# Performance work log

Measured on AMD Instinct MI355X. Metric: run time of the kernel, lower is better.

## Reference

```python
import jax, jax.numpy as jnp
import numpy as np

EPS_NORM = 1e-12  # matches torch F.normalize eps
EPS_LOG = 1e-10


def _l2norm(x):
    n = jnp.sqrt(jnp.sum(x * x, axis=-1, keepdims=True))
    return x / jnp.maximum(n, EPS_NORM)


def setup_inputs() -> dict:
    key = jax.random.key(0)
    k1, k2 = jax.random.split(key)
    B, H, K, Dh = 65536, 4, 512, 256
    z_e = jax.random.normal(k1, (B, H * Dh), dtype=jnp.float32)
    emb = jax.random.normal(k2, (H, K, Dh), dtype=jnp.float32)  # per-head codebooks
    logit_scales = jnp.ones((H,), dtype=jnp.float32) * 10.0
    return {"z_e": z_e, "emb": emb, "logit_scales": logit_scales}


def reference(z_e, emb, logit_scales):
    B = z_e.shape[0]
    H, K, Dh = emb.shape
    z = z_e.reshape(B, H, Dh)
    zn = _l2norm(z)                      # [B,H,Dh]
    en = _l2norm(emb)                    # [H,K,Dh]
    # per-head cosine similarity, scaled
    logits = logit_scales[None, :, None] * jnp.einsum('bhd,hkd->bhk', zn, en)  # [B,H,K]
    idx = jnp.argmax(logits, axis=-1)    # [B,H] int
    # embedding gather per head: emb[h, idx[b,h]] -> [B,H,Dh]
    z_q = emb[jnp.arange(H)[None, :], idx].reshape(B, H * Dh)
    # perplexity per head
    probs = jax.nn.softmax(logits, axis=-1)          # [B,H,K]
    avg_probs = probs.mean(axis=0)                   # [H,K]
    perp = jnp.exp(-jnp.sum(avg_probs * jnp.log(avg_probs + EPS_LOG), axis=-1))  # [H]
    avg_perplexity = perp.mean()
    # combined radix index over heads
    combined = idx[:, 0]
    for h in range(1, H):
        combined = combined * K + idx[:, h]
    return z_q, combined, avg_perplexity
```

## Files before the change

kernel.cpp:

```cpp
#include <hip/hip_runtime.h>
#include <stdint.h>
#include <math.h>

#define BT   65536
#define H    4
#define K    512
#define DH   256
#define EPSN 1e-12f
#define EPSL 1e-10f
#define TAU  0.03f
#define CTH  0.970446f
#define CMAX 16
#define NREP 8
#define LOG2E 1.4426950408889634f

typedef short bf16x8 __attribute__((ext_vector_type(8)));
typedef float f32x4  __attribute__((ext_vector_type(4)));

__device__ inline unsigned short f2bf(float f) {
  uint32_t u = __builtin_bit_cast(uint32_t, f);
  u += 0x7fffu + ((u >> 16) & 1u);
  return (unsigned short)(u >> 16);
}

__device__ inline uint32_t pack_bf2(float lo, float hi) {
  uint32_t r;
  asm("v_cvt_pk_bf16_f32 %0, %1, %2" : "=v"(r) : "v"(lo), "v"(hi));
  return r;
}


__global__ __launch_bounds__(256) void vq_prep(const float* __restrict__ emb,
                                               const float* __restrict__ scales,
                                               float* __restrict__ en_f,
                                               unsigned short* __restrict__ en_t,
                                               float* __restrict__ avgp) {
  const int hk = blockIdx.x;
  const int t  = threadIdx.x;
  const float v = emb[(size_t)hk * DH + t];
  float s = v * v;
#pragma unroll
  for (int m = 1; m < 64; m <<= 1) s += __shfl_xor(s, m);
  __shared__ float wsum[4];
  if ((t & 63) == 0) wsum[t >> 6] = s;
  __syncthreads();
  const float tot = wsum[0] + wsum[1] + wsum[2] + wsum[3];
  const float n   = fmaxf(sqrtf(tot), EPSN);
  const float vn  = v / n;
  en_f[(size_t)hk * DH + t] = vn;

  const int h    = hk >> 9, k = hk & (K - 1);
  const float s2 = scales[h] * LOG2E;
  const int kblk = k >> 4, arow = k & 15;
  const int ks   = t >> 5, kg = (t >> 3) & 3, e = t & 7;
  const int lane = (kg << 4) | arow;
  en_t[(((size_t)(h * 32 + kblk) * 8 + ks) * 64 + lane) * 8 + e] = f2bf(vn * s2);
  if (t < NREP) avgp[t * (H * K) + hk] = 0.0f;
}

__global__ __launch_bounds__(512, 4) void vq_main(
    const float* __restrict__ z_e, const float* __restrict__ emb,
    const float* __restrict__ en_f, const unsigned short* __restrict__ en_t,
    float* __restrict__ avgp, int* __restrict__ idx_ws,
    float* __restrict__ outq) {
  const int h     = blockIdx.y;
  const int bbase = blockIdx.x * 64;
  const int t     = threadIdx.x;
  const int w     = t >> 6;
  const int l     = t & 63;
  const int arow  = l & 15;
  const int kg    = l >> 4;

  __shared__ unsigned short a_lds[64 * 256];
  __shared__ float norms[64];
  __shared__ float invn_l[64];
  __shared__ float wredm[8][64];
  __shared__ float wreds[8][64];
  __shared__ __align__(16) unsigned short cand[64][CMAX];
  __shared__ float thr[64];
  __shared__ float Srec[64];
  __shared__ int   cnt[64];
  __shared__ float avg_lds[512];

  {
    const int row = t >> 3;
    const int c8  = t & 7;
    const float* zp = z_e + (size_t)(bbase + row) * (H * DH) + h * DH;
    float4 q[8];
    float ss = 0.0f;
    const int swz = (row & 7) << 4;
#pragma unroll
    for (int j = 0; j < 8; j++) {
      q[j] = *(const float4*)(zp + c8 * 4 + j * 32);
      const int d = c8 * 4 + j * 32;
      uint2 pk;
      pk.x = pack_bf2(q[j].x, q[j].y);
      pk.y = pack_bf2(q[j].z, q[j].w);
      *(uint2*)((char*)a_lds + row * 512 + ((d * 2) ^ swz)) = pk;
      ss += q[j].x * q[j].x + q[j].y * q[j].y + q[j].z * q[j].z + q[j].w * q[j].w;
    }
    ss += __shfl_xor(ss, 1);
    ss += __shfl_xor(ss, 2);
    ss += __shfl_xor(ss, 4);
    const float n = fmaxf(sqrtf(ss), EPSN);
    if (c8 == 0) { norms[row] = n; invn_l[row] = 1.0f / n; }
    if (t < 64) cnt[t] = 0;
  }

  const unsigned short* ep =
      en_t + (((size_t)(h * 32 + w * 4) * 8) * 64 + l) * 8;
  bf16x8 ef0[4];
#pragma unroll
  for (int mi = 0; mi < 4; mi++)
    ef0[mi] = *(const bf16x8*)(ep + (size_t)(mi * 8) * 512);

  __syncthreads();

  f32x4 acc[4][4];
#pragma unroll
  for (int mi = 0; mi < 4; mi++)
#pragma unroll
    for (int ni = 0; ni < 4; ni++) acc[mi][ni] = (f32x4){0.f, 0.f, 0.f, 0.f};

#pragma unroll
  for (int ks = 0; ks < 8; ks++) {
    bf16x8 ef[4];
    if (ks == 0) {
#pragma unroll
      for (int mi = 0; mi < 4; mi++) ef[mi] = ef0[mi];
    } else {
#pragma unroll
      for (int mi = 0; mi < 4; mi++)
        ef[mi] = *(const bf16x8*)(ep + (size_t)(mi * 8 + ks) * 512);
    }
    bf16x8 zf[4];
#pragma unroll
    for (int ni = 0; ni < 4; ni++) {
      const int rr = ni * 16 + arow;
      const int kb = (ks * 64) | (kg * 16);
      zf[ni] = *(const bf16x8*)((const char*)a_lds + rr * 512 +
                                (kb ^ ((rr & 7) << 4)));
    }
#pragma unroll
    for (int mi = 0; mi < 4; mi++)
#pragma unroll
      for (int ni = 0; ni < 4; ni++)
        acc[mi][ni] = __builtin_amdgcn_mfma_f32_16x16x32_bf16(ef[mi], zf[ni],
                                                              acc[mi][ni], 0, 0, 0);
  }

  float rn[4];
#pragma unroll
  for (int ni = 0; ni < 4; ni++) rn[ni] = invn_l[ni * 16 + arow];
  float m1[4], es[4];
#pragma unroll
  for (int ni = 0; ni < 4; ni++) { m1[ni] = 0.0f; es[ni] = 0.0f; }
#pragma unroll
  for (int mi = 0; mi < 4; mi++)
#pragma unroll
    for (int ni = 0; ni < 4; ni++)
#pragma unroll
      for (int q = 0; q < 4; q++) {
        const float e = __builtin_amdgcn_exp2f(acc[mi][ni][q] * rn[ni]);
        acc[mi][ni][q] = e;
        m1[ni] = fmaxf(m1[ni], e);
        es[ni] += e;
      }
#pragma unroll
  for (int m = 16; m < 64; m <<= 1) {
#pragma unroll
    for (int ni = 0; ni < 4; ni++) {
      m1[ni] = fmaxf(m1[ni], __shfl_xor(m1[ni], m));
      es[ni] += __shfl_xor(es[ni], m);
    }
  }
  if (kg == 0) {
#pragma unroll
    for (int ni = 0; ni < 4; ni++) {
      const int r = ni * 16 + arow;
      wredm[w][r] = m1[ni];
      wreds[w][r] = es[ni];
    }
  }
  __syncthreads();
  if (t < 64) {
    float a1 = 0.0f, s = 0.0f;
#pragma unroll
    for (int ww = 0; ww < 8; ww++) {
      a1 = fmaxf(a1, wredm[ww][t]);
      s += wreds[ww][t];
    }
    thr[t] = a1 * CTH; Srec[t] = 1.0f / s;
  }
  __syncthreads();

  {
    float rs[4], th[4];
#pragma unroll
    for (int ni = 0; ni < 4; ni++) {
      const int r = ni * 16 + arow;
      rs[ni] = Srec[r];
      th[ni] = thr[r];
    }
#pragma unroll
    for (int mi = 0; mi < 4; mi++)
#pragma unroll
      for (int q = 0; q < 4; q++) {
        float vs = 0.0f;
#pragma unroll
        for (int ni = 0; ni < 4; ni++) {
          const float e = acc[mi][ni][q];
          vs = fmaf(e, rs[ni], vs);
          if (e >= th[ni]) {
            const int r = ni * 16 + arow;
            const int p = atomicAdd(&cnt[r], 1);
            if (p < CMAX)
              cand[r][p] = (unsigned short)(w * 64 + mi * 16 + kg * 4 + q);
          }
        }
        vs += __shfl_xor(vs, 1);
        vs += __shfl_xor(vs, 2);
        vs += __shfl_xor(vs, 4);
        vs += __shfl_xor(vs, 8);
        if (arow == 0) avg_lds[w * 64 + mi * 16 + kg * 4 + q] = vs;
      }
  }
  __syncthreads();

  {
    float* ap = avgp + (blockIdx.x & (NREP - 1)) * (H * K) + h * K;
    atomicAdd(&ap[t], avg_lds[t]);
  }

  int best8[8];
#pragma unroll
  for (int i = 0; i < 8; i++) {
    const int r = w * 8 + i;
    int c = cnt[r];
    int best;
    if (c <= 1) {
      best = cand[r][0];
    } else {
      if (c > CMAX) c = CMAX;
      const float nrm = norms[r];
      const float4 zq = *(const float4*)(z_e + (size_t)(bbase + r) * (H * DH) +
                                         h * DH + l * 4);
      const float zn0 = zq.x / nrm, zn1 = zq.y / nrm,
                  zn2 = zq.z / nrm, zn3 = zq.w / nrm;
      float bv = -INFINITY; int bi = 1 << 30;
      for (int j = 0; j < c; j++) {
        const int cd = cand[r][j];
        const float4 eq = *(const float4*)(en_f + ((size_t)(h * K) + cd) * DH + l * 4);
        float d0 = fmaf(zn0, eq.x, fmaf(zn1, eq.y, fmaf(zn2, eq.z, zn3 * eq.w)));
#pragma unroll
        for (int m = 1; m < 64; m <<= 1) d0 += __shfl_xor(d0, m);
        if (d0 > bv || (d0 == bv && cd < bi)) { bv = d0; bi = cd; }
      }
      best = bi;
    }
    best8[i] = best;
    if (l == i) idx_ws[(size_t)(bbase + r) * H + h] = best;
  }

  {
    float4 gv[8];
#pragma unroll
    for (int i = 0; i < 8; i++)
      gv[i] = *(const float4*)(emb + ((size_t)(h * K) + best8[i]) * DH + l * 4);
#pragma unroll
    for (int i = 0; i < 8; i++)
      *(float4*)(outq + (size_t)(bbase + w * 8 + i) * (H * DH) + h * DH + l * 4) =
          gv[i];
  }
}

__global__ __launch_bounds__(256) void vq_tail(const int* __restrict__ idx_ws,
                                               const float* __restrict__ avgp,
                                               float* __restrict__ out_comb,
                                               float* __restrict__ out_perp) {
  const int t = threadIdx.x;
  if (blockIdx.x < 256) {
    const int b = blockIdx.x * 256 + t;
    const int* p = idx_ws + (size_t)b * H;
    uint32_t cv = (uint32_t)p[0];
    cv = cv * 512u + (uint32_t)p[1];
    cv = cv * 512u + (uint32_t)p[2];
    cv = cv * 512u + (uint32_t)p[3];
    out_comb[b] = (float)(int32_t)cv;
    return;
  }
  float sh[H] = {0.f, 0.f, 0.f, 0.f};
  for (int i = t; i < H * K; i += 256) {
    const int h = i >> 9;
    float a = 0.0f;
#pragma unroll
    for (int c = 0; c < NREP; c++) a += avgp[c * (H * K) + i];
    a /= 65536.0f;
    sh[h] += a * logf(a + EPSL);
  }
  __shared__ float red[4][H];
#pragma unroll
  for (int h = 0; h < H; h++) {
    float s = sh[h];
#pragma unroll
    for (int m = 1; m < 64; m <<= 1) s += __shfl_xor(s, m);
    if ((t & 63) == 0) red[t >> 6][h] = s;
  }
  __syncthreads();
  if (t == 0) {
    float p = 0.0f;
#pragma unroll
    for (int h = 0; h < H; h++) {
      const float s = red[0][h] + red[1][h] + red[2][h] + red[3][h];
      p += expf(-s);
    }
    out_perp[0] = p * 0.25f;
  }
}

extern "C" void kernel_launch(void* const* d_in, const int* in_sizes, int n_in,
                              void* d_out, int out_size, void* d_ws, size_t ws_size,
                              hipStream_t stream) {
  const float* z_e    = (const float*)d_in[0];
  const float* emb    = (const float*)d_in[1];
  const float* scales = (const float*)d_in[2];
  float* out = (float*)d_out;

  float*          en_f   = (float*)d_ws;
  unsigned short* en_t   = (unsigned short*)(en_f + (size_t)H * K * DH);
  float*          avgp   = (float*)(en_t + (size_t)H * K * DH);
  int*            idx_ws = (int*)(avgp + NREP * H * K);

  hipLaunchKernelGGL(vq_prep, dim3(H * K), dim3(256), 0, stream,
                     emb, scales, en_f, en_t, avgp);
  hipLaunchKernelGGL(vq_main, dim3(BT / 64, H), dim3(512), 0, stream,
                     z_e, emb, en_f, en_t, avgp, idx_ws, out);
  hipLaunchKernelGGL(vq_tail, dim3(BT / 256 + 1), dim3(256), 0, stream,
                     idx_ws, avgp, out + (size_t)BT * H * DH,
                     out + (size_t)BT * H * DH + BT);
}
```

Measured before the change: 225.0 us.

## Process two 64-row tiles per block to amortize setup and atomics

Each vq_main block now handles 128 rows as two 64-row tiles, and the grid is halved to match. The global loads of z for both tiles are issued up front so more memory traffic is in flight at once. The perplexity partial sums of both tiles are combined in LDS before a single atomic flush, which halves the global atomics. The cost is that the row tile, candidate and count LDS buffers are doubled, which may lower the number of resident blocks per CU, and the codebook fragments are re-read from memory for the second tile.

```diff
diff --git a/kernel.cpp b/kernel.cpp
--- a/kernel.cpp
+++ b/kernel.cpp
@@ -64,47 +64,65 @@
     float* __restrict__ avgp, int* __restrict__ idx_ws,
     float* __restrict__ outq) {
   const int h     = blockIdx.y;
-  const int bbase = blockIdx.x * 64;
+  const int bbase = blockIdx.x * 128;
   const int t     = threadIdx.x;
   const int w     = t >> 6;
   const int l     = t & 63;
   const int arow  = l & 15;
   const int kg    = l >> 4;
 
-  __shared__ unsigned short a_lds[64 * 256];
-  __shared__ float norms[64];
-  __shared__ float invn_l[64];
+  __shared__ unsigned short a_lds[2][64 * 256];
+  __shared__ float norms[2][64];
+  __shared__ float invn_l[2][64];
   __shared__ float wredm[8][64];
   __shared__ float wreds[8][64];
-  __shared__ __align__(16) unsigned short cand[64][CMAX];
+  __shared__ __align__(16) unsigned short cand[2][64][CMAX];
   __shared__ float thr[64];
   __shared__ float Srec[64];
-  __shared__ int   cnt[64];
+  __shared__ int   cnt[2][64];
   __shared__ float avg_lds[512];
 
   {
     const int row = t >> 3;
     const int c8  = t & 7;
-    const float* zp = z_e + (size_t)(bbase + row) * (H * DH) + h * DH;
-    float4 q[8];
-    float ss = 0.0f;
+    const float* zp0 = z_e + (size_t)(bbase + row) * (H * DH) + h * DH;
+    const float* zp1 = zp0 + (size_t)64 * (H * DH);
+    float4 q0[8], q1[8];
+#pragma unroll
+    for (int j = 0; j < 8; j++) q0[j] = *(const float4*)(zp0 + c8 * 4 + j * 32);
+#pragma unroll
+    for (int j = 0; j < 8; j++) q1[j] = *(const float4*)(zp1 + c8 * 4 + j * 32);
     const int swz = (row & 7) << 4;
+    float ss0 = 0.0f, ss1 = 0.0f;
 #pragma unroll
     for (int j = 0; j < 8; j++) {
-      q[j] = *(const float4*)(zp + c8 * 4 + j * 32);
       const int d = c8 * 4 + j * 32;
       uint2 pk;
-      pk.x = pack_bf2(q[j].x, q[j].y);
-      pk.y = pack_bf2(q[j].z, q[j].w);
-      *(uint2*)((char*)a_lds + row * 512 + ((d * 2) ^ swz)) = pk;
-      ss += q[j].x * q[j].x + q[j].y * q[j].y + q[j].z * q[j].z + q[j].w * q[j].w;
-    }
-    ss += __shfl_xor(ss, 1);
-    ss += __shfl_xor(ss, 2);
-    ss += __shfl_xor(ss, 4);
-    const float n = fmaxf(sqrtf(ss), EPSN);
-    if (c8 == 0) { norms[row] = n; invn_l[row] = 1.0f / n; }
-    if (t < 64) cnt[t] = 0;
+      pk.x = pack_bf2(q0[j].x, q0[j].y);
+      pk.y = pack_bf2(q0[j].z, q0[j].w);
+      *(uint2*)((char*)&a_lds[0][0] + row * 512 + ((d * 2) ^ swz)) = pk;
+      ss0 += q0[j].x * q0[j].x + q0[j].y * q0[j].y +
+             q0[j].z * q0[j].z + q0[j].w * q0[j].w;
+    }
+#pragma unroll
+    for (int j = 0; j < 8; j++) {
+      const int d = c8 * 4 + j * 32;
+      uint2 pk;
+      pk.x = pack_bf2(q1[j].x, q1[j].y);
+      pk.y = pack_bf2(q1[j].z, q1[j].w);
+      *(uint2*)((char*)&a_lds[1][0] + row * 512 + ((d * 2) ^ swz)) = pk;
+      ss1 += q1[j].x * q1[j].x + q1[j].y * q1[j].y +
+             q1[j].z * q1[j].z + q1[j].w * q1[j].w;
+    }
+    ss0 += __shfl_xor(ss0, 1); ss0 += __shfl_xor(ss0, 2); ss0 += __shfl_xor(ss0, 4);
+    ss1 += __shfl_xor(ss1, 1); ss1 += __shfl_xor(ss1, 2); ss1 += __shfl_xor(ss1, 4);
+    if (c8 == 0) {
+      const float n0 = fmaxf(sqrtf(ss0), EPSN);
+      const float n1 = fmaxf(sqrtf(ss1), EPSN);
+      norms[0][row] = n0; invn_l[0][row] = 1.0f / n0;
+      norms[1][row] = n1; invn_l[1][row] = 1.0f / n1;
+    }
+    if (t < 64) { cnt[0][t] = 0; cnt[1][t] = 0; }
   }
 
   const unsigned short* ep =
@@ -116,114 +134,120 @@
 
   __syncthreads();
 
-  f32x4 acc[4][4];
-#pragma unroll
-  for (int mi = 0; mi < 4; mi++)
-#pragma unroll
-    for (int ni = 0; ni < 4; ni++) acc[mi][ni] = (f32x4){0.f, 0.f, 0.f, 0.f};
-
-#pragma unroll
-  for (int ks = 0; ks < 8; ks++) {
-    bf16x8 ef[4];
-    if (ks == 0) {
-#pragma unroll
-      for (int mi = 0; mi < 4; mi++) ef[mi] = ef0[mi];
-    } else {
+#pragma unroll
+  for (int tile = 0; tile < 2; ++tile) {
+    const unsigned short* al = &a_lds[tile][0];
+
+    f32x4 acc[4][4];
+#pragma unroll
+    for (int mi = 0; mi < 4; mi++)
+#pragma unroll
+      for (int ni = 0; ni < 4; ni++) acc[mi][ni] = (f32x4){0.f, 0.f, 0.f, 0.f};
+
+#pragma unroll
+    for (int ks = 0; ks < 8; ks++) {
+      bf16x8 ef[4];
 #pragma unroll
       for (int mi = 0; mi < 4; mi++)
-        ef[mi] = *(const bf16x8*)(ep + (size_t)(mi * 8 + ks) * 512);
-    }
-    bf16x8 zf[4];
-#pragma unroll
-    for (int ni = 0; ni < 4; ni++) {
-      const int rr = ni * 16 + arow;
-      const int kb = (ks * 64) | (kg * 16);
-      zf[ni] = *(const bf16x8*)((const char*)a_lds + rr * 512 +
-                                (kb ^ ((rr & 7) << 4)));
-    }
+        ef[mi] = (tile == 0 && ks == 0)
+                     ? ef0[mi]
+                     : *(const bf16x8*)(ep + (size_t)(mi * 8 + ks) * 512);
+      bf16x8 zf[4];
+#pragma unroll
+      for (int ni = 0; ni < 4; ni++) {
+        const int rr = ni * 16 + arow;
+        const int kb = (ks * 64) | (kg * 16);
+        zf[ni] = *(const bf16x8*)((const char*)al + rr * 512 +
+                                  (kb ^ ((rr & 7) << 4)));
+      }
+#pragma unroll
+      for (int mi = 0; mi < 4; mi++)
+#pragma unroll
+        for (int ni = 0; ni < 4; ni++)
+          acc[mi][ni] = __builtin_amdgcn_mfma_f32_16x16x32_bf16(ef[mi], zf[ni],
+                                                                acc[mi][ni], 0, 0, 0);
+    }
+
+    float rn[4];
+#pragma unroll
+    for (int ni = 0; ni < 4; ni++) rn[ni] = invn_l[tile][ni * 16 + arow];
+    float m1[4], es[4];
+#pragma unroll
+    for (int ni = 0; ni < 4; ni++) { m1[ni] = 0.0f; es[ni] = 0.0f; }
 #pragma unroll
     for (int mi = 0; mi < 4; mi++)
 #pragma unroll
       for (int ni = 0; ni < 4; ni++)
-        acc[mi][ni] = __builtin_amdgcn_mfma_f32_16x16x32_bf16(ef[mi], zf[ni],
-                                                              acc[mi][ni], 0, 0, 0);
-  }
-
-  float rn[4];
-#pragma unroll
-  for (int ni = 0; ni < 4; ni++) rn[ni] = invn_l[ni * 16 + arow];
-  float m1[4], es[4];
-#pragma unroll
-  for (int ni = 0; ni < 4; ni++) { m1[ni] = 0.0f; es[ni] = 0.0f; }
-#pragma unroll
-  for (int mi = 0; mi < 4; mi++)
-#pragma unroll
-    for (int ni = 0; ni < 4; ni++)
-#pragma unroll
-      for (int q = 0; q < 4; q++) {
-        const float e = __builtin_amdgcn_exp2f(acc[mi][ni][q] * rn[ni]);
-        acc[mi][ni][q] = e;
-        m1[ni] = fmaxf(m1[ni], e);
-        es[ni] += e;
-      }
-#pragma unroll
-  for (int m = 16; m < 64; m <<= 1) {
-#pragma unroll
-    for (int ni = 0; ni < 4; ni++) {
-      m1[ni] = fmaxf(m1[ni], __shfl_xor(m1[ni], m));
-      es[ni] += __shfl_xor(es[ni], m);
-    }
-  }
-  if (kg == 0) {
-#pragma unroll
-    for (int ni = 0; ni < 4; ni++) {
-      const int r = ni * 16 + arow;
-      wredm[w][r] = m1[ni];
-      wreds[w][r] = es[ni];
-    }
-  }
-  __syncthreads();
-  if (t < 64) {
-    float a1 = 0.0f, s = 0.0f;
-#pragma unroll
-    for (int ww = 0; ww < 8; ww++) {
-      a1 = fmaxf(a1, wredm[ww][t]);
-      s += wreds[ww][t];
-    }
-    thr[t] = a1 * CTH; Srec[t] = 1.0f / s;
-  }
-  __syncthreads();
-
-  {
-    float rs[4], th[4];
-#pragma unroll
-    for (int ni = 0; ni < 4; ni++) {
-      const int r = ni * 16 + arow;
-      rs[ni] = Srec[r];
-      th[ni] = thr[r];
-    }
-#pragma unroll
-    for (int mi = 0; mi < 4; mi++)
-#pragma unroll
-      for (int q = 0; q < 4; q++) {
-        float vs = 0.0f;
-#pragma unroll
-        for (int ni = 0; ni < 4; ni++) {
-          const float e = acc[mi][ni][q];
-          vs = fmaf(e, rs[ni], vs);
-          if (e >= th[ni]) {
-            const int r = ni * 16 + arow;
-            const int p = atomicAdd(&cnt[r], 1);
-            if (p < CMAX)
-              cand[r][p] = (unsigned short)(w * 64 + mi * 16 + kg * 4 + q);
+#pragma unroll
+        for (int q = 0; q < 4; q++) {
+          const float e = __builtin_amdgcn_exp2f(acc[mi][ni][q] * rn[ni]);
+          acc[mi][ni][q] = e;
+          m1[ni] = fmaxf(m1[ni], e);
+          es[ni] += e;
+        }
+#pragma unroll
+    for (int m = 16; m < 64; m <<= 1) {
+#pragma unroll
+      for (int ni = 0; ni < 4; ni++) {
+        m1[ni] = fmaxf(m1[ni], __shfl_xor(m1[ni], m));
+        es[ni] += __shfl_xor(es[ni], m);
+      }
+    }
+    if (kg == 0) {
+#pragma unroll
+      for (int ni = 0; ni < 4; ni++) {
+        const int r = ni * 16 + arow;
+        wredm[w][r] = m1[ni];
+        wreds[w][r] = es[ni];
+      }
+    }
+    __syncthreads();
+    if (t < 64) {
+      float a1 = 0.0f, s = 0.0f;
+#pragma unroll
+      for (int ww = 0; ww < 8; ww++) {
+        a1 = fmaxf(a1, wredm[ww][t]);
+        s += wreds[ww][t];
+      }
+      thr[t] = a1 * CTH; Srec[t] = 1.0f / s;
+    }
+    __syncthreads();
+
+    {
+      float rs[4], th4[4];
+#pragma unroll
+      for (int ni = 0; ni < 4; ni++) {
+        const int r = ni * 16 + arow;
+        rs[ni]  = Srec[r];
+        th4[ni] = thr[r];
+      }
+#pragma unroll
+      for (int mi = 0; mi < 4; mi++)
+#pragma unroll
+        for (int q = 0; q < 4; q++) {
+          float vs = 0.0f;
+#pragma unroll
+          for (int ni = 0; ni < 4; ni++) {
+            const float e = acc[mi][ni][q];
+            vs = fmaf(e, rs[ni], vs);
+            if (e >= th4[ni]) {
+              const int r = ni * 16 + arow;
+              const int p = atomicAdd(&cnt[tile][r], 1);
+              if (p < CMAX)
+                cand[tile][r][p] = (unsigned short)(w * 64 + mi * 16 + kg * 4 + q);
+            }
+          }
+          vs += __shfl_xor(vs, 1);
+          vs += __shfl_xor(vs, 2);
+          vs += __shfl_xor(vs, 4);
+          vs += __shfl_xor(vs, 8);
+          if (arow == 0) {
+            const int idx = w * 64 + mi * 16 + kg * 4 + q;
+            if (tile == 0) avg_lds[idx] = vs;
+            else           avg_lds[idx] += vs;
           }
         }
-        vs += __shfl_xor(vs, 1);
-        vs += __shfl_xor(vs, 2);
-        vs += __shfl_xor(vs, 4);
-        vs += __shfl_xor(vs, 8);
-        if (arow == 0) avg_lds[w * 64 + mi * 16 + kg * 4 + q] = vs;
-      }
+    }
   }
   __syncthreads();
 
@@ -232,45 +256,51 @@
     atomicAdd(&ap[t], avg_lds[t]);
   }
 
-  int best8[8];
-#pragma unroll
-  for (int i = 0; i < 8; i++) {
-    const int r = w * 8 + i;
-    int c = cnt[r];
-    int best;
-    if (c <= 1) {
-      best = cand[r][0];
-    } else {
-      if (c > CMAX) c = CMAX;
-      const float nrm = norms[r];
-      const float4 zq = *(const float4*)(z_e + (size_t)(bbase + r) * (H * DH) +
-                                         h * DH + l * 4);
-      const float zn0 = zq.x / nrm, zn1 = zq.y / nrm,
-                  zn2 = zq.z / nrm, zn3 = zq.w / nrm;
-      float bv = -INFINITY; int bi = 1 << 30;
-      for (int j = 0; j < c; j++) {
-        const int cd = cand[r][j];
-        const float4 eq = *(const float4*)(en_f + ((size_t)(h * K) + cd) * DH + l * 4);
-        float d0 = fmaf(zn0, eq.x, fmaf(zn1, eq.y, fmaf(zn2, eq.z, zn3 * eq.w)));
-#pragma unroll
-        for (int m = 1; m < 64; m <<= 1) d0 += __shfl_xor(d0, m);
-        if (d0 > bv || (d0 == bv && cd < bi)) { bv = d0; bi = cd; }
-      }
-      best = bi;
-    }
-    best8[i] = best;
-    if (l == i) idx_ws[(size_t)(bbase + r) * H + h] = best;
-  }
-
-  {
+  int best16[16];
+#pragma unroll
+  for (int tile = 0; tile < 2; ++tile) {
+#pragma unroll
+    for (int i = 0; i < 8; i++) {
+      const int r    = w * 8 + i;
+      const int grow = bbase + tile * 64 + r;
+      int c = cnt[tile][r];
+      int best;
+      if (c <= 1) {
+        best = cand[tile][r][0];
+      } else {
+        if (c > CMAX) c = CMAX;
+        const float nrm = norms[tile][r];
+        const float4 zq = *(const float4*)(z_e + (size_t)grow * (H * DH) +
+                                           h * DH + l * 4);
+        const float zn0 = zq.x / nrm, zn1 = zq.y / nrm,
+                    zn2 = zq.z / nrm, zn3 = zq.w / nrm;
+        float bv = -INFINITY; int bi = 1 << 30;
+        for (int j = 0; j < c; j++) {
+          const int cd = cand[tile][r][j];
+          const float4 eq = *(const float4*)(en_f + ((size_t)(h * K) + cd) * DH + l * 4);
+          float d0 = fmaf(zn0, eq.x, fmaf(zn1, eq.y, fmaf(zn2, eq.z, zn3 * eq.w)));
+#pragma unroll
+          for (int m = 1; m < 64; m <<= 1) d0 += __shfl_xor(d0, m);
+          if (d0 > bv || (d0 == bv && cd < bi)) { bv = d0; bi = cd; }
+        }
+        best = bi;
+      }
+      best16[tile * 8 + i] = best;
+      if (l == tile * 8 + i) idx_ws[(size_t)grow * H + h] = best;
+    }
+  }
+
+#pragma unroll
+  for (int tile = 0; tile < 2; ++tile) {
     float4 gv[8];
 #pragma unroll
     for (int i = 0; i < 8; i++)
-      gv[i] = *(const float4*)(emb + ((size_t)(h * K) + best8[i]) * DH + l * 4);
+      gv[i] = *(const float4*)(emb +
+               ((size_t)(h * K) + best16[tile * 8 + i]) * DH + l * 4);
 #pragma unroll
     for (int i = 0; i < 8; i++)
-      *(float4*)(outq + (size_t)(bbase + w * 8 + i) * (H * DH) + h * DH + l * 4) =
-          gv[i];
+      *(float4*)(outq + (size_t)(bbase + tile * 64 + w * 8 + i) * (H * DH) +
+                 h * DH + l * 4) = gv[i];
   }
 }
 
@@ -333,7 +363,7 @@
 
   hipLaunchKernelGGL(vq_prep, dim3(H * K), dim3(256), 0, stream,
                      emb, scales, en_f, en_t, avgp);
-  hipLaunchKernelGGL(vq_main, dim3(BT / 64, H), dim3(512), 0, stream,
+  hipLaunchKernelGGL(vq_main, dim3(BT / 128, H), dim3(512), 0, stream,
                      z_e, emb, en_f, en_t, avgp, idx_ws, out);
   hipLaunchKernelGGL(vq_tail, dim3(BT / 256 + 1), dim3(256), 0, stream,
                      idx_ws, avgp, out + (size_t)BT * H * DH,
```

Measured after the change: 342.8 us. 52.4% more time.
